# Performance work log

Hardware: AMD Instinct MI355X
Metric: run time of the kernel (lower is better)

## Reference

```python
import jax, jax.numpy as jnp
import numpy as np
import math

B, T, C = 4, 1024, 1024
N_HEAD = 16
HEAD_DIM = C // N_HEAD


def alibi_slopes(n_head):
    # standard ALiBi slopes for power-of-2 head counts: 2^(-8*i/n), i=1..n
    start = 2.0 ** (-8.0 / n_head)
    return jnp.asarray([start ** (i + 1) for i in range(n_head)], dtype=jnp.float32)


def alibi_bias(n_head, t):
    # encoder (is_decoder=False): symmetric bias -slope * |i - j|, shape [1, H, T, T]
    pos = jnp.arange(t)
    dist = -jnp.abs(pos[None, :] - pos[:, None]).astype(jnp.float32)  # [T, T]
    return (alibi_slopes(n_head)[:, None, None] * dist)[None]  # [1, H, T, T]


def setup_inputs() -> dict:
    key = jax.random.key(0)
    ks = jax.random.split(key, 5)
    s = 1.0 / math.sqrt(C)
    return {
        "x": jax.random.normal(ks[0], (B, T, C), dtype=jnp.float32),
        "Wq": jax.random.normal(ks[1], (C, C), dtype=jnp.float32) * s,
        "Wk": jax.random.normal(ks[2], (C, C), dtype=jnp.float32) * s,
        "Wv": jax.random.normal(ks[3], (C, C), dtype=jnp.float32) * s,
        "Wp": jax.random.normal(ks[4], (C, C), dtype=jnp.float32) * s,
    }


def reference(x, Wq, Wk, Wv, Wp):
    b, t, c = x.shape
    h, d = N_HEAD, HEAD_DIM
    # torch nn.Linear(bias=False): y = x @ W.T
    q = (x @ Wq.T).reshape(b, t, h, d).transpose(0, 2, 1, 3)  # [B,H,T,D]
    k = (x @ Wk.T).reshape(b, t, h, d).transpose(0, 2, 1, 3)
    v = (x @ Wv.T).reshape(b, t, h, d).transpose(0, 2, 1, 3)
    scores = jnp.einsum('bhqd,bhkd->bhqk', q, k) * (1.0 / math.sqrt(d))
    scores = scores + alibi_bias(h, t).astype(scores.dtype)
    attn = jax.nn.softmax(scores, axis=-1)  # [B,H,T,T]
    y = jnp.einsum('bhqk,bhkd->bhqd', attn, v)
    y = y.transpose(0, 2, 1, 3).reshape(b, t, c)
    y = y @ Wp.T
    return (y, attn)
```

## Files before the change

kernel.cpp:

```cpp
#include <hip/hip_runtime.h>
#include <hip/hip_bf16.h>


typedef _Float16 half8 __attribute__((ext_vector_type(8)));
typedef _Float16 half4 __attribute__((ext_vector_type(4)));
typedef float f32x4 __attribute__((ext_vector_type(4)));

#define MFMA16(a, b, c) __builtin_amdgcn_mfma_f32_16x16x32_f16((a), (b), (c), 0, 0, 0)

__global__ __launch_bounds__(256) void cvt_kernel(const float* __restrict__ src,
                                                  _Float16* __restrict__ dst, int n4) {
  int i = blockIdx.x * 256 + threadIdx.x;
  if (i < n4) {
    float4 v = ((const float4*)src)[i];
    half4 o = {(_Float16)v.x, (_Float16)v.y, (_Float16)v.z, (_Float16)v.w};
    *(half4*)&dst[(size_t)i * 4] = o;
  }
}

__device__ __forceinline__ void stage_tile(const _Float16* gbase, _Float16* lds, int tid) {
#pragma unroll
  for (int i = 0; i < 2; ++i) {
    int cid = i * 256 + tid;
    int row = cid >> 2, jl = cid & 3;
    int jg = jl ^ (row & 3);
    const _Float16* gp = gbase + (size_t)row * 1024 + jg * 8;
    _Float16* lp = lds + (size_t)cid * 8;
    __builtin_amdgcn_global_load_lds(
        (const __attribute__((address_space(1))) unsigned int*)gp,
        (__attribute__((address_space(3))) unsigned int*)lp, 16, 0, 0);
  }
}

__device__ __forceinline__ void gemm_core(const _Float16* __restrict__ A,
                                          const _Float16* __restrict__ B,
                                          int m0, int n0, int tid,
                                          f32x4 (&acc)[4][4]) {
  __shared__ _Float16 As[128 * 32];
  __shared__ _Float16 Bs[128 * 32];
  const int wave = tid >> 6, lane = tid & 63;
  const int wr = wave >> 1, wc = wave & 1;
  const int lg = lane >> 4, lm = lane & 15;

  f32x4 z4 = {0.f, 0.f, 0.f, 0.f};
#pragma unroll
  for (int mt = 0; mt < 4; ++mt)
#pragma unroll
    for (int nt = 0; nt < 4; ++nt) acc[mt][nt] = z4;

  for (int kb = 0; kb < 32; ++kb) {
    stage_tile(A + (size_t)m0 * 1024 + kb * 32, As, tid);
    stage_tile(B + (size_t)n0 * 1024 + kb * 32, Bs, tid);
    __syncthreads();
    half8 af[4], bf[4];
#pragma unroll
    for (int mt = 0; mt < 4; ++mt) {
      int row = wr * 64 + mt * 16 + lm;
      int ch = lg ^ (row & 3);
      af[mt] = *(half8*)&As[row * 32 + ch * 8];
    }
#pragma unroll
    for (int nt = 0; nt < 4; ++nt) {
      int row = wc * 64 + nt * 16 + lm;
      int ch = lg ^ (row & 3);
      bf[nt] = *(half8*)&Bs[row * 32 + ch * 8];
    }
#pragma unroll
    for (int mt = 0; mt < 4; ++mt)
#pragma unroll
      for (int nt = 0; nt < 4; ++nt)
        acc[mt][nt] = MFMA16(af[mt], bf[nt], acc[mt][nt]);
    __syncthreads();
  }
}

__global__ __launch_bounds__(256) void qkv_gemm(
    const _Float16* __restrict__ x16, const _Float16* __restrict__ wq,
    const _Float16* __restrict__ wk, const _Float16* __restrict__ wv,
    _Float16* __restrict__ qo, _Float16* __restrict__ ko, _Float16* __restrict__ vo) {
  const int tid = threadIdx.x;
  const int z = blockIdx.z;
  const _Float16* W = (z == 0) ? wq : (z == 1) ? wk : wv;
  const int m0 = blockIdx.y * 128, n0 = blockIdx.x * 128;
  const int wave = tid >> 6, lane = tid & 63;
  const int wr = wave >> 1, wc = wave & 1;
  const int lg = lane >> 4, lm = lane & 15;

  f32x4 acc[4][4];
  gemm_core(x16, W, m0, n0, tid, acc);

  if (z == 2) {
#pragma unroll
    for (int mt = 0; mt < 4; ++mt) {
      int mbase = m0 + wr * 64 + mt * 16 + lg * 4;
      int b = mbase >> 10, t = mbase & 1023;
#pragma unroll
      for (int nt = 0; nt < 4; ++nt) {
        int n = n0 + wc * 64 + nt * 16 + lm;
        int h = n >> 6, d = n & 63;
        half4 o;
#pragma unroll
        for (int r = 0; r < 4; ++r) o[r] = (_Float16)acc[mt][nt][r];
        *(half4*)&vo[(((size_t)(b * 16 + h) * 64 + d) << 10) + t] = o;
      }
    }
  } else {
    _Float16* dst = (z == 0) ? qo : ko;
    const float s = (z == 0) ? 0.125f : 1.0f;
#pragma unroll
    for (int mt = 0; mt < 4; ++mt) {
      int mbase = m0 + wr * 64 + mt * 16 + lg * 4;
      int b = mbase >> 10, t = mbase & 1023;
#pragma unroll
      for (int nt = 0; nt < 4; ++nt) {
        int n = n0 + wc * 64 + nt * 16 + lm;
        int h = n >> 6, d = n & 63;
#pragma unroll
        for (int r = 0; r < 4; ++r)
          dst[((size_t)(b * 16 + h) * 1024 + t + r) * 64 + d] =
              (_Float16)(acc[mt][nt][r] * s);
      }
    }
  }
}

__global__ __launch_bounds__(512) void attn_fused(
    const _Float16* __restrict__ qg, const _Float16* __restrict__ kg,
    const _Float16* __restrict__ vg, float* __restrict__ attn,
    _Float16* __restrict__ y16) {
  const int bh = blockIdx.y;
  const int b = bh >> 4, h = bh & 15;
  const int q0 = blockIdx.x << 5;
  const int tid = threadIdx.x;
  const int wave = tid >> 6, lane = tid & 63;
  const int wr = wave >> 2, wc = wave & 3;
  const int lg = lane >> 4, lm = lane & 15;

  __shared__ _Float16 q_lds[32 * 72];
  __shared__ _Float16 p_lds[8 * 16 * 40];
  __shared__ float red[4][32];
  __shared__ float o_red[2][4][16 * 64];

  if (tid < 256) {
    int r = tid >> 3, c = tid & 7;
    *(half8*)&q_lds[r * 72 + c * 8] =
        *(const half8*)&qg[((size_t)bh * 1024 + q0 + r) * 64 + c * 8];
  }
  __syncthreads();

  f32x4 z4 = {0.f, 0.f, 0.f, 0.f};
  f32x4 acc[16];
#pragma unroll
  for (int i = 0; i < 16; ++i) acc[i] = z4;

  const int arow = wr * 16 + lm;
  half8 a0 = *(half8*)&q_lds[arow * 72 + lg * 8];
  half8 a1 = *(half8*)&q_lds[arow * 72 + 32 + lg * 8];
  const _Float16* kbase = kg + ((size_t)bh << 16);
#pragma unroll
  for (int nt = 0; nt < 16; ++nt) {
    int n = wc * 256 + nt * 16 + lm;
    half8 b0 = *(const half8*)&kbase[(size_t)n * 64 + lg * 8];
    half8 b1 = *(const half8*)&kbase[(size_t)n * 64 + 32 + lg * 8];
    acc[nt] = MFMA16(a0, b0, acc[nt]);
    acc[nt] = MFMA16(a1, b1, acc[nt]);
  }

  const float slope = exp2f(-0.5f * (float)(h + 1));
  const int qrow0 = q0 + wr * 16 + lg * 4;
  float mx[4] = {-1e30f, -1e30f, -1e30f, -1e30f};
#pragma unroll
  for (int nt = 0; nt < 16; ++nt) {
    int col = wc * 256 + nt * 16 + lm;
#pragma unroll
    for (int r = 0; r < 4; ++r) {
      float v = acc[nt][r] - slope * fabsf((float)(qrow0 + r - col));
      acc[nt][r] = v;
      mx[r] = fmaxf(mx[r], v);
    }
  }
#pragma unroll
  for (int r = 0; r < 4; ++r)
#pragma unroll
    for (int d = 1; d < 16; d <<= 1) mx[r] = fmaxf(mx[r], __shfl_xor(mx[r], d, 64));
  if (lm == 0) {
#pragma unroll
    for (int r = 0; r < 4; ++r) red[wc][wr * 16 + lg * 4 + r] = mx[r];
  }
  __syncthreads();
  float m[4];
#pragma unroll
  for (int r = 0; r < 4; ++r) {
    int row = wr * 16 + lg * 4 + r;
    m[r] = fmaxf(fmaxf(red[0][row], red[1][row]), fmaxf(red[2][row], red[3][row]));
  }
  __syncthreads();

  float sm[4] = {0.f, 0.f, 0.f, 0.f};
#pragma unroll
  for (int nt = 0; nt < 16; ++nt)
#pragma unroll
    for (int r = 0; r < 4; ++r) {
      float p = exp2f((acc[nt][r] - m[r]) * 1.4426950408889634f);
      acc[nt][r] = p;
      sm[r] += p;
    }
#pragma unroll
  for (int r = 0; r < 4; ++r)
#pragma unroll
    for (int d = 1; d < 16; d <<= 1) sm[r] += __shfl_xor(sm[r], d, 64);
  if (lm == 0) {
#pragma unroll
    for (int r = 0; r < 4; ++r) red[wc][wr * 16 + lg * 4 + r] = sm[r];
  }
  __syncthreads();
  float inv[4];
#pragma unroll
  for (int r = 0; r < 4; ++r) {
    int row = wr * 16 + lg * 4 + r;
    inv[r] = 1.0f / (red[0][row] + red[1][row] + red[2][row] + red[3][row]);
  }

  float* abase = attn + ((size_t)bh << 20);
#pragma unroll
  for (int nt = 0; nt < 16; ++nt) {
    int col = wc * 256 + nt * 16 + lm;
#pragma unroll
    for (int r = 0; r < 4; ++r) {
      float pn = acc[nt][r] * inv[r];
      acc[nt][r] = pn;
      abase[((size_t)(qrow0 + r) << 10) + col] = pn;
    }
  }

  f32x4 oacc[4];
#pragma unroll
  for (int i = 0; i < 4; ++i) oacc[i] = z4;
  _Float16* pl = &p_lds[wave * 640];
  const _Float16* vbase = vg + ((size_t)bh << 16);
#pragma unroll
  for (int c = 0; c < 8; ++c) {
#pragma unroll
    for (int hv = 0; hv < 2; ++hv)
#pragma unroll
      for (int r = 0; r < 4; ++r)
        pl[(lg * 4 + r) * 40 + hv * 16 + lm] = (_Float16)acc[2 * c + hv][r];
    half8 pa = *(half8*)&pl[lm * 40 + lg * 8];
    int kk = wc * 256 + c * 32 + lg * 8;
#pragma unroll
    for (int dt = 0; dt < 4; ++dt) {
      half8 vb = *(const half8*)&vbase[(size_t)(dt * 16 + lm) * 1024 + kk];
      oacc[dt] = MFMA16(pa, vb, oacc[dt]);
    }
  }

#pragma unroll
  for (int dt = 0; dt < 4; ++dt)
#pragma unroll
    for (int r = 0; r < 4; ++r)
      o_red[wr][wc][(lg * 4 + r) * 64 + dt * 16 + lm] = oacc[dt][r];
  __syncthreads();
#pragma unroll
  for (int it = 0; it < 4; ++it) {
    int idx = tid + it * 512;
    int row = idx >> 6, col = idx & 63;
    int r2 = row & 15, wrr = row >> 4;
    float s = o_red[wrr][0][r2 * 64 + col] + o_red[wrr][1][r2 * 64 + col] +
              o_red[wrr][2][r2 * 64 + col] + o_red[wrr][3][r2 * 64 + col];
    y16[((size_t)(b * 1024 + q0 + row)) * 1024 + h * 64 + col] = (_Float16)s;
  }
}

__global__ __launch_bounds__(256) void proj_gemm(const _Float16* __restrict__ y16,
                                                 const _Float16* __restrict__ wp,
                                                 float* __restrict__ out) {
  const int tid = threadIdx.x;
  const int m0 = blockIdx.y * 128, n0 = blockIdx.x * 128;
  const int wave = tid >> 6, lane = tid & 63;
  const int wr = wave >> 1, wc = wave & 1;
  const int lg = lane >> 4, lm = lane & 15;

  f32x4 acc[4][4];
  gemm_core(y16, wp, m0, n0, tid, acc);

#pragma unroll
  for (int mt = 0; mt < 4; ++mt) {
    int mbase = m0 + wr * 64 + mt * 16 + lg * 4;
#pragma unroll
    for (int nt = 0; nt < 4; ++nt) {
      int n = n0 + wc * 64 + nt * 16 + lm;
#pragma unroll
      for (int r = 0; r < 4; ++r)
        out[(size_t)(mbase + r) * 1024 + n] = acc[mt][nt][r];
    }
  }
}

extern "C" void kernel_launch(void* const* d_in, const int* in_sizes, int n_in,
                              void* d_out, int out_size, void* d_ws, size_t ws_size,
                              hipStream_t stream) {
  const float* x = (const float*)d_in[0];
  const float* Wq = (const float*)d_in[1];
  const float* Wk = (const float*)d_in[2];
  const float* Wv = (const float*)d_in[3];
  const float* Wp = (const float*)d_in[4];
  float* out = (float*)d_out;

  char* ws = (char*)d_ws;
  _Float16* x16 = (_Float16*)(ws);
  _Float16* wq16 = (_Float16*)(ws + (8u << 20));
  _Float16* wk16 = (_Float16*)(ws + (10u << 20));
  _Float16* wv16 = (_Float16*)(ws + (12u << 20));
  _Float16* wp16 = (_Float16*)(ws + (14u << 20));
  _Float16* q16 = (_Float16*)(ws + (16u << 20));
  _Float16* k16 = (_Float16*)(ws + (24u << 20));
  _Float16* v16 = (_Float16*)(ws + (32u << 20));
  _Float16* y16 = (_Float16*)(ws + (40u << 20));

  cvt_kernel<<<4096, 256, 0, stream>>>(x, x16, 1048576);
  cvt_kernel<<<1024, 256, 0, stream>>>(Wq, wq16, 262144);
  cvt_kernel<<<1024, 256, 0, stream>>>(Wk, wk16, 262144);
  cvt_kernel<<<1024, 256, 0, stream>>>(Wv, wv16, 262144);
  cvt_kernel<<<1024, 256, 0, stream>>>(Wp, wp16, 262144);

  qkv_gemm<<<dim3(8, 32, 3), 256, 0, stream>>>(x16, wq16, wk16, wv16, q16, k16, v16);
  attn_fused<<<dim3(32, 64), 512, 0, stream>>>(q16, k16, v16, out + 4194304, y16);
  proj_gemm<<<dim3(8, 32, 1), 256, 0, stream>>>(y16, wp16, out);
}
```

Before: 505.1 us.

## Fuse conversion launches, deepen GEMM K-tile, add nontemporal stores and occupancy hint

The five fp16 conversion launches are merged into one kernel that dispatches on the global index. The shared GEMM core now stages 64-wide K tiles with an 8-way XOR swizzle, halving the loop trips and barriers. The attention probability writes and the projection output writes become nontemporal stores, and attn_fused gets a min-blocks launch bound of 4. The larger LDS tiles and the launch-bound hint may cut occupancy or cause register spills.

```diff
diff --git a/kernel.cpp b/kernel.cpp
--- a/kernel.cpp
+++ b/kernel.cpp
@@ -8,22 +8,36 @@
 
 #define MFMA16(a, b, c) __builtin_amdgcn_mfma_f32_16x16x32_f16((a), (b), (c), 0, 0, 0)
 
-__global__ __launch_bounds__(256) void cvt_kernel(const float* __restrict__ src,
-                                                  _Float16* __restrict__ dst, int n4) {
+__global__ __launch_bounds__(256) void cvt_all(
+    const float* __restrict__ x, const float* __restrict__ wq,
+    const float* __restrict__ wk, const float* __restrict__ wv,
+    const float* __restrict__ wp, _Float16* __restrict__ x16,
+    _Float16* __restrict__ wq16, _Float16* __restrict__ wk16,
+    _Float16* __restrict__ wv16, _Float16* __restrict__ wp16) {
   int i = blockIdx.x * 256 + threadIdx.x;
-  if (i < n4) {
-    float4 v = ((const float4*)src)[i];
-    half4 o = {(_Float16)v.x, (_Float16)v.y, (_Float16)v.z, (_Float16)v.w};
-    *(half4*)&dst[(size_t)i * 4] = o;
-  }
+  const float* src;
+  _Float16* dst;
+  int off;
+  if (i < 1048576) {
+    src = x; dst = x16; off = i;
+  } else {
+    int j = i - 1048576;
+    int sel = j >> 18;
+    off = j & 262143;
+    src = (sel == 0) ? wq : (sel == 1) ? wk : (sel == 2) ? wv : wp;
+    dst = (sel == 0) ? wq16 : (sel == 1) ? wk16 : (sel == 2) ? wv16 : wp16;
+  }
+  float4 v = ((const float4*)src)[off];
+  half4 o = {(_Float16)v.x, (_Float16)v.y, (_Float16)v.z, (_Float16)v.w};
+  *(half4*)&dst[(size_t)off * 4] = o;
 }
 
 __device__ __forceinline__ void stage_tile(const _Float16* gbase, _Float16* lds, int tid) {
 #pragma unroll
-  for (int i = 0; i < 2; ++i) {
+  for (int i = 0; i < 4; ++i) {
     int cid = i * 256 + tid;
-    int row = cid >> 2, jl = cid & 3;
-    int jg = jl ^ (row & 3);
+    int row = cid >> 3, jl = cid & 7;
+    int jg = jl ^ (row & 7);
     const _Float16* gp = gbase + (size_t)row * 1024 + jg * 8;
     _Float16* lp = lds + (size_t)cid * 8;
     __builtin_amdgcn_global_load_lds(
@@ -36,8 +50,8 @@
                                           const _Float16* __restrict__ B,
                                           int m0, int n0, int tid,
                                           f32x4 (&acc)[4][4]) {
-  __shared__ _Float16 As[128 * 32];
-  __shared__ _Float16 Bs[128 * 32];
+  __shared__ _Float16 As[128 * 64];
+  __shared__ _Float16 Bs[128 * 64];
   const int wave = tid >> 6, lane = tid & 63;
   const int wr = wave >> 1, wc = wave & 1;
   const int lg = lane >> 4, lm = lane & 15;
@@ -48,28 +62,31 @@
 #pragma unroll
     for (int nt = 0; nt < 4; ++nt) acc[mt][nt] = z4;
 
-  for (int kb = 0; kb < 32; ++kb) {
-    stage_tile(A + (size_t)m0 * 1024 + kb * 32, As, tid);
-    stage_tile(B + (size_t)n0 * 1024 + kb * 32, Bs, tid);
+  for (int kb = 0; kb < 16; ++kb) {
+    stage_tile(A + (size_t)m0 * 1024 + kb * 64, As, tid);
+    stage_tile(B + (size_t)n0 * 1024 + kb * 64, Bs, tid);
     __syncthreads();
-    half8 af[4], bf[4];
-#pragma unroll
-    for (int mt = 0; mt < 4; ++mt) {
-      int row = wr * 64 + mt * 16 + lm;
-      int ch = lg ^ (row & 3);
-      af[mt] = *(half8*)&As[row * 32 + ch * 8];
-    }
-#pragma unroll
-    for (int nt = 0; nt < 4; ++nt) {
-      int row = wc * 64 + nt * 16 + lm;
-      int ch = lg ^ (row & 3);
-      bf[nt] = *(half8*)&Bs[row * 32 + ch * 8];
-    }
-#pragma unroll
-    for (int mt = 0; mt < 4; ++mt)
-#pragma unroll
-      for (int nt = 0; nt < 4; ++nt)
-        acc[mt][nt] = MFMA16(af[mt], bf[nt], acc[mt][nt]);
+#pragma unroll
+    for (int h = 0; h < 2; ++h) {
+      half8 af[4], bf[4];
+#pragma unroll
+      for (int mt = 0; mt < 4; ++mt) {
+        int row = wr * 64 + mt * 16 + lm;
+        int ch = (lg + h * 4) ^ (row & 7);
+        af[mt] = *(half8*)&As[row * 64 + ch * 8];
+      }
+#pragma unroll
+      for (int nt = 0; nt < 4; ++nt) {
+        int row = wc * 64 + nt * 16 + lm;
+        int ch = (lg + h * 4) ^ (row & 7);
+        bf[nt] = *(half8*)&Bs[row * 64 + ch * 8];
+      }
+#pragma unroll
+      for (int mt = 0; mt < 4; ++mt)
+#pragma unroll
+        for (int nt = 0; nt < 4; ++nt)
+          acc[mt][nt] = MFMA16(af[mt], bf[nt], acc[mt][nt]);
+    }
     __syncthreads();
   }
 }
@@ -124,7 +141,7 @@
   }
 }
 
-__global__ __launch_bounds__(512) void attn_fused(
+__global__ __launch_bounds__(512, 4) void attn_fused(
     const _Float16* __restrict__ qg, const _Float16* __restrict__ kg,
     const _Float16* __restrict__ vg, float* __restrict__ attn,
     _Float16* __restrict__ y16) {
@@ -229,7 +246,7 @@
     for (int r = 0; r < 4; ++r) {
       float pn = acc[nt][r] * inv[r];
       acc[nt][r] = pn;
-      abase[((size_t)(qrow0 + r) << 10) + col] = pn;
+      __builtin_nontemporal_store(pn, &abase[((size_t)(qrow0 + r) << 10) + col]);
     }
   }
 
@@ -291,7 +308,8 @@
       int n = n0 + wc * 64 + nt * 16 + lm;
 #pragma unroll
       for (int r = 0; r < 4; ++r)
-        out[(size_t)(mbase + r) * 1024 + n] = acc[mt][nt][r];
+        __builtin_nontemporal_store(acc[mt][nt][r],
+                                    &out[(size_t)(mbase + r) * 1024 + n]);
     }
   }
 }
@@ -317,11 +335,7 @@
   _Float16* v16 = (_Float16*)(ws + (32u << 20));
   _Float16* y16 = (_Float16*)(ws + (40u << 20));
 
-  cvt_kernel<<<4096, 256, 0, stream>>>(x, x16, 1048576);
-  cvt_kernel<<<1024, 256, 0, stream>>>(Wq, wq16, 262144);
-  cvt_kernel<<<1024, 256, 0, stream>>>(Wk, wk16, 262144);
-  cvt_kernel<<<1024, 256, 0, stream>>>(Wv, wv16, 262144);
-  cvt_kernel<<<1024, 256, 0, stream>>>(Wp, wp16, 262144);
+  cvt_all<<<8192, 256, 0, stream>>>(x, Wq, Wk, Wv, Wp, x16, wq16, wk16, wv16, wp16);
 
   qkv_gemm<<<dim3(8, 32, 3), 256, 0, stream>>>(x16, wq16, wk16, wv16, q16, k16, v16);
   attn_fused<<<dim3(32, 64), 512, 0, stream>>>(q16, k16, v16, out + 4194304, y16);
```

New measurement: 466.8 us. -7.6%, faster.
